# Performance work log

Hardware: AMD Instinct MI355X
Metric: run time of the kernel (lower is better)

Reference implementation:

```python
import jax, jax.numpy as jnp
import numpy as np


def setup_inputs() -> dict:
    key = jax.random.key(0)
    k1, k2, k3, k4 = jax.random.split(key, 4)
    B, C, H, W = 4, 48, 512, 512
    T, ws = 3, 64
    # factor matrices (per TensorMultiplication_einsum, T summation terms)
    # init scale: 1/(init_temperature**(1/3) * sqrt(out_dim)) with init_temperature=1.0
    Ws = jax.random.normal(k2, (T, ws, ws), jnp.float32) / np.sqrt(ws)
    Hs = jax.random.normal(k3, (T, ws, ws), jnp.float32) / np.sqrt(ws)
    Cs = jax.random.normal(k4, (T, C, C), jnp.float32) / np.sqrt(C)
    x = jax.random.normal(k1, (B, C, H, W), jnp.float32)
    return {"x": x, "Ws": Ws, "Hs": Hs, "Cs": Cs, "window_size": ws}


def reference(x, Ws, Hs, Cs, window_size):
    """FeatureProcessingBlock forward:
      window_partition -> sum_t einsum('bchw,wW,hH,cC->bCHW') -> window_reverse.
    The window partition/reverse reshapes are fused into one einsum over the
    blocked view (p,q index the window grid; h,w index within-window pixels).
    """
    B, C, H, W = x.shape
    ws = window_size
    # (B, C, H//ws, ws, W//ws, ws)
    xb = x.reshape(B, C, H // ws, ws, W // ws, ws)
    # sum over T terms and contract w, h, c axes with their factor matrices
    out = jnp.einsum('bcphqw,twW,thH,tcC->bCpHqW', xb, Ws, Hs, Cs)
    return out.reshape(B, C, H, W)
```

## Files before the change

### kernel.cpp

```cpp
#include <hip/hip_runtime.h>
#include <hip/hip_bf16.h>


typedef __attribute__((ext_vector_type(8))) short short8;
typedef __attribute__((ext_vector_type(4))) short short4v;
typedef __attribute__((ext_vector_type(4))) float float4v;

#define SMEM_BYTES 161296

static __device__ __forceinline__ unsigned short f2bf(float f) {
  return __builtin_bit_cast(unsigned short, __float2bfloat16(f));
}
static __device__ __forceinline__ unsigned int pk2(float a, float b) {
  return (unsigned int)f2bf(a) | ((unsigned int)f2bf(b) << 16);
}
static __device__ __forceinline__ void wg_barrier_lds() {
  asm volatile("s_waitcnt lgkmcnt(0)" ::: "memory");
  __builtin_amdgcn_s_barrier();
  asm volatile("" ::: "memory");
}

__global__ __launch_bounds__(512, 2)
void fpb13(const float* __restrict__ x, const float* __restrict__ Ws,
           const float* __restrict__ Hsm, const float* __restrict__ Cs,
           float* __restrict__ out) {
  extern __shared__ char smem[];
  char* Y1F = smem;
  char* Zb  = smem + 49152;
  char* Cf  = smem + 147456;
  char* z16 = smem + 161280;

  int wid = (blockIdx.x & 7) * 128 + (blockIdx.x >> 3);
  int window = wid >> 2, tile = wid & 3;
  int b = window >> 6, p = (window >> 3) & 7, q = window & 7;
  int j0 = tile * 16;

  int tid = threadIdx.x, lane = tid & 63, wave = tid >> 6;
  int lq = lane >> 4, lc = lane & 15;
  int clA = wave & 3, hh = wave >> 2;
  int mt  = wave & 3, cp = wave >> 2;

  if (tid < 4) ((unsigned int*)z16)[tid] = 0;

  for (int idx = wave; idx < 18; idx += 8) {
    int ss = idx / 3, m = idx - 3 * ss;
    if (lq < 3) {
      short8 v;
      #pragma unroll
      for (int e = 0; e < 8; ++e)
        v[e] = (short)f2bf(Cs[lq * 2304 + (8 * ss + e) * 48 + 16 * m + lc]);
      *(short8*)(Cf + (idx * 16 + lc) * 48 + lq * 16) = v;
    }
  }

  short8 wsf[3][2], hsf[3][2];
  #pragma unroll
  for (int t = 0; t < 3; ++t)
    #pragma unroll
    for (int sv = 0; sv < 2; ++sv) {
      short8 aa, bb;
      #pragma unroll
      for (int e = 0; e < 8; ++e) {
        int k = 32 * sv + 8 * lq + e;
        aa[e] = (short)f2bf(Ws [t * 4096 + k * 64 + j0 + lc]);
        bb[e] = (short)f2bf(Hsm[t * 4096 + k * 64 + 16 * mt + lc]);
      }
      wsf[t][sv] = aa; hsf[t][sv] = bb;
    }

  float4v acc[3][8];
  #pragma unroll
  for (int m = 0; m < 3; ++m)
    #pragma unroll
    for (int i = 0; i < 8; ++i) acc[m][i] = float4v{0.f, 0.f, 0.f, 0.f};

  const float* xA = x + (((size_t)b * 48) * 512 + p * 64) * 512 + q * 64
                      + (size_t)clA * 262144 + (size_t)(32 * hh + lc) * 512 + 8 * lq;

  float4v fin[8];
  #define LOADFIN(vv) do {                                        \
    const float* srcb_ = xA + (size_t)(vv) * 1048576;             \
    _Pragma("unroll")                                             \
    for (int j2_ = 0; j2_ < 2; ++j2_) {                           \
      const float* r_ = srcb_ + (size_t)j2_ * 8192;               \
      fin[4*j2_+0] = *(const float4v*)(r_);                       \
      fin[4*j2_+1] = *(const float4v*)(r_ + 4);                   \
      fin[4*j2_+2] = *(const float4v*)(r_ + 32);                  \
      fin[4*j2_+3] = *(const float4v*)(r_ + 36);                  \
    }                                                             \
  } while (0)

  #define ABLOCK(vv) do {                                                     \
    char* yb_ = Y1F + ((vv) & 1) * 24576;                                     \
    short8 af_[4];                                                            \
    _Pragma("unroll")                                                         \
    for (int j2_ = 0; j2_ < 2; ++j2_) {                                       \
      short8 a0_, a1_;                                                        \
      _Pragma("unroll")                                                       \
      for (int e2_ = 0; e2_ < 4; ++e2_) {                                     \
        a0_[e2_]   = (short)f2bf(fin[4*j2_+0][e2_]);                          \
        a0_[4+e2_] = (short)f2bf(fin[4*j2_+1][e2_]);                          \
        a1_[e2_]   = (short)f2bf(fin[4*j2_+2][e2_]);                          \
        a1_[4+e2_] = (short)f2bf(fin[4*j2_+3][e2_]);                          \
      }                                                                       \
      af_[2*j2_] = a0_; af_[2*j2_+1] = a1_;                                   \
    }                                                                         \
    if ((vv) < 11) LOADFIN((vv) + 1);                                         \
    _Pragma("unroll")                                                         \
    for (int j2_ = 0; j2_ < 2; ++j2_) {                                       \
      int mA_  = 2 * hh + j2_;                                                \
      int sv_  = mA_ >> 1;                                                    \
      int lqp_ = (2 * mA_ + (lq >> 1)) & 3;                                   \
      int eo_  = (lq & 1) * 8;                                                \
      _Pragma("unroll")                                                       \
      for (int t_ = 0; t_ < 3; ++t_) {                                        \
        float4v d_ = {0.f, 0.f, 0.f, 0.f};                                    \
        d_ = __builtin_amdgcn_mfma_f32_16x16x32_bf16(af_[2*j2_],   wsf[t_][0], d_, 0, 0, 0); \
        d_ = __builtin_amdgcn_mfma_f32_16x16x32_bf16(af_[2*j2_+1], wsf[t_][1], d_, 0, 0, 0); \
        short4v pv_;                                                          \
        pv_[0] = (short)f2bf(d_[0]); pv_[1] = (short)f2bf(d_[1]);             \
        pv_[2] = (short)f2bf(d_[2]); pv_[3] = (short)f2bf(d_[3]);             \
        *(short4v*)(yb_ + ((t_ * 4 + clA) * 2 + sv_) * 1024                   \
                        + (lqp_ * 16 + lc) * 16 + eo_) = pv_;                 \
      }                                                                       \
    }                                                                         \
  } while (0)

  LOADFIN(0);
  wg_barrier_lds();
  ABLOCK(0);
  wg_barrier_lds();

  #pragma unroll 1
  for (int v = 0; v < 12; ++v) {
    {
      const char* yb = Y1F + (v & 1) * 24576;
      char* zb = Zb + ((v >> 1) & 1) * 49152;
      int half = (v & 1) * 8;
      #pragma unroll
      for (int t = 0; t < 3; ++t) {
        float4v dB[2];
        #pragma unroll
        for (int cj = 0; cj < 2; ++cj) {
          int cl = 2 * cp + cj;
          const char* ybs = yb + ((t * 4 + cl) * 2) * 1024 + lane * 16;
          short8 y0 = *(const short8*)ybs;
          short8 y1 = *(const short8*)(ybs + 1024);
          float4v dd = {0.f, 0.f, 0.f, 0.f};
          dd = __builtin_amdgcn_mfma_f32_16x16x32_bf16(hsf[t][0], y0, dd, 0, 0, 0);
          dd = __builtin_amdgcn_mfma_f32_16x16x32_bf16(hsf[t][1], y1, dd, 0, 0, 0);
          dB[cj] = dd;
        }
        #pragma unroll
        for (int r = 0; r < 4; ++r) {
          int px = (16 * mt + 4 * lq + r) * 16 + lc;
          *(unsigned int*)(zb + t * 16384 + px * 16 + half + 4 * cp) =
              pk2(dB[0][r], dB[1][r]);
        }
      }
    }
    if (v < 11) ABLOCK(v + 1);
    if ((v & 1) && v >= 3) {
      int Sp = (v >> 1) - 1;
      const char* zb = Zb + (Sp & 1) * 49152;
      short8 cf[3];
      #pragma unroll
      for (int m = 0; m < 3; ++m) {
        const char* csrc = (lq < 3) ? (Cf + ((Sp * 3 + m) * 16 + lc) * 48 + lq * 16) : z16;
        cf[m] = *(const short8*)csrc;
      }
      #pragma unroll
      for (int i = 0; i < 8; ++i) {
        int px = 16 * (wave + 8 * i) + lc;
        const char* zsrc = (lq < 3) ? (zb + lq * 16384 + px * 16) : z16;
        short8 zf = *(const short8*)zsrc;
        acc[0][i] = __builtin_amdgcn_mfma_f32_16x16x32_bf16(cf[0], zf, acc[0][i], 0, 0, 0);
        acc[1][i] = __builtin_amdgcn_mfma_f32_16x16x32_bf16(cf[1], zf, acc[1][i], 0, 0, 0);
        acc[2][i] = __builtin_amdgcn_mfma_f32_16x16x32_bf16(cf[2], zf, acc[2][i], 0, 0, 0);
      }
    }
    wg_barrier_lds();
  }

  {
    const char* zb = Zb + 1 * 49152;
    short8 cf[3];
    #pragma unroll
    for (int m = 0; m < 3; ++m) {
      const char* csrc = (lq < 3) ? (Cf + ((5 * 3 + m) * 16 + lc) * 48 + lq * 16) : z16;
      cf[m] = *(const short8*)csrc;
    }
    #pragma unroll
    for (int i = 0; i < 8; ++i) {
      int px = 16 * (wave + 8 * i) + lc;
      const char* zsrc = (lq < 3) ? (zb + lq * 16384 + px * 16) : z16;
      short8 zf = *(const short8*)zsrc;
      acc[0][i] = __builtin_amdgcn_mfma_f32_16x16x32_bf16(cf[0], zf, acc[0][i], 0, 0, 0);
      acc[1][i] = __builtin_amdgcn_mfma_f32_16x16x32_bf16(cf[1], zf, acc[1][i], 0, 0, 0);
      acc[2][i] = __builtin_amdgcn_mfma_f32_16x16x32_bf16(cf[2], zf, acc[2][i], 0, 0, 0);
    }
  }

  #pragma unroll
  for (int m = 0; m < 3; ++m)
    #pragma unroll
    for (int i = 0; i < 8; ++i) {
      int n = wave + 8 * i;
      size_t rowbase = (((size_t)(b * 48 + 16 * m + 4 * lq)) * 512 + p * 64 + n) * 512
                       + q * 64 + j0 + lc;
      #pragma unroll
      for (int r = 0; r < 4; ++r)
        out[rowbase + (size_t)r * 262144] = acc[m][i][r];
    }
}

extern "C" void kernel_launch(void* const* d_in, const int* in_sizes, int n_in,
                              void* d_out, int out_size, void* d_ws, size_t ws_size,
                              hipStream_t stream) {
  (void)in_sizes; (void)n_in; (void)d_ws; (void)ws_size; (void)out_size;
  const float* x   = (const float*)d_in[0];
  const float* Ws  = (const float*)d_in[1];
  const float* Hsm = (const float*)d_in[2];
  const float* Cs  = (const float*)d_in[3];
  float* out = (float*)d_out;
  (void)hipFuncSetAttribute((const void*)fpb13,
                            hipFuncAttributeMaxDynamicSharedMemorySize, SMEM_BYTES);
  fpb13<<<dim3(1024), dim3(512), SMEM_BYTES, stream>>>(x, Ws, Hsm, Cs, out);
}
```

Measured before the change: 191.2 us.

## Warp-specialize waves into W-stage producers and H-stage consumers with 8-channel chunks

Splits the workgroup so waves 0-3 do the H contraction and waves 4-7 do the global load plus W contraction. Each step now handles 8 channels instead of 4, with a single Z buffer and doubled Y1 buffers. All waves still run the C contraction after a barrier. The aim is to overlap the global loads and first-stage MFMA work with the second stage while halving the number of barrier-synchronized steps. The cost is an uneven per-wave workload, more registers for the doubled fin buffers, and role-split waves sharing barriers, which may serialize work instead of overlapping it.

```diff
diff --git a/kernel.cpp b/kernel.cpp
--- a/kernel.cpp
+++ b/kernel.cpp
@@ -10,9 +10,6 @@
 
 static __device__ __forceinline__ unsigned short f2bf(float f) {
   return __builtin_bit_cast(unsigned short, __float2bfloat16(f));
-}
-static __device__ __forceinline__ unsigned int pk2(float a, float b) {
-  return (unsigned int)f2bf(a) | ((unsigned int)f2bf(b) << 16);
 }
 static __device__ __forceinline__ void wg_barrier_lds() {
   asm volatile("s_waitcnt lgkmcnt(0)" ::: "memory");
@@ -21,12 +18,12 @@
 }
 
 __global__ __launch_bounds__(512, 2)
-void fpb13(const float* __restrict__ x, const float* __restrict__ Ws,
+void fpb14(const float* __restrict__ x, const float* __restrict__ Ws,
            const float* __restrict__ Hsm, const float* __restrict__ Cs,
            float* __restrict__ out) {
   extern __shared__ char smem[];
   char* Y1F = smem;
-  char* Zb  = smem + 49152;
+  char* Zb  = smem + 98304;
   char* Cf  = smem + 147456;
   char* z16 = smem + 161280;
 
@@ -37,8 +34,6 @@
 
   int tid = threadIdx.x, lane = tid & 63, wave = tid >> 6;
   int lq = lane >> 4, lc = lane & 15;
-  int clA = wave & 3, hh = wave >> 2;
-  int mt  = wave & 3, cp = wave >> 2;
 
   if (tid < 4) ((unsigned int*)z16)[tid] = 0;
 
@@ -53,151 +48,158 @@
     }
   }
 
-  short8 wsf[3][2], hsf[3][2];
-  #pragma unroll
-  for (int t = 0; t < 3; ++t)
-    #pragma unroll
-    for (int sv = 0; sv < 2; ++sv) {
-      short8 aa, bb;
-      #pragma unroll
-      for (int e = 0; e < 8; ++e) {
-        int k = 32 * sv + 8 * lq + e;
-        aa[e] = (short)f2bf(Ws [t * 4096 + k * 64 + j0 + lc]);
-        bb[e] = (short)f2bf(Hsm[t * 4096 + k * 64 + 16 * mt + lc]);
-      }
-      wsf[t][sv] = aa; hsf[t][sv] = bb;
-    }
-
   float4v acc[3][8];
   #pragma unroll
   for (int m = 0; m < 3; ++m)
     #pragma unroll
     for (int i = 0; i < 8; ++i) acc[m][i] = float4v{0.f, 0.f, 0.f, 0.f};
 
-  const float* xA = x + (((size_t)b * 48) * 512 + p * 64) * 512 + q * 64
-                      + (size_t)clA * 262144 + (size_t)(32 * hh + lc) * 512 + 8 * lq;
-
-  float4v fin[8];
-  #define LOADFIN(vv) do {                                        \
-    const float* srcb_ = xA + (size_t)(vv) * 1048576;             \
-    _Pragma("unroll")                                             \
-    for (int j2_ = 0; j2_ < 2; ++j2_) {                           \
-      const float* r_ = srcb_ + (size_t)j2_ * 8192;               \
-      fin[4*j2_+0] = *(const float4v*)(r_);                       \
-      fin[4*j2_+1] = *(const float4v*)(r_ + 4);                   \
-      fin[4*j2_+2] = *(const float4v*)(r_ + 32);                  \
-      fin[4*j2_+3] = *(const float4v*)(r_ + 36);                  \
-    }                                                             \
-  } while (0)
-
-  #define ABLOCK(vv) do {                                                     \
-    char* yb_ = Y1F + ((vv) & 1) * 24576;                                     \
-    short8 af_[4];                                                            \
+  #define CBLOCK(s_) do {                                                     \
+    short8 cf_[3];                                                            \
     _Pragma("unroll")                                                         \
-    for (int j2_ = 0; j2_ < 2; ++j2_) {                                       \
-      short8 a0_, a1_;                                                        \
-      _Pragma("unroll")                                                       \
-      for (int e2_ = 0; e2_ < 4; ++e2_) {                                     \
-        a0_[e2_]   = (short)f2bf(fin[4*j2_+0][e2_]);                          \
-        a0_[4+e2_] = (short)f2bf(fin[4*j2_+1][e2_]);                          \
-        a1_[e2_]   = (short)f2bf(fin[4*j2_+2][e2_]);                          \
-        a1_[4+e2_] = (short)f2bf(fin[4*j2_+3][e2_]);                          \
-      }                                                                       \
-      af_[2*j2_] = a0_; af_[2*j2_+1] = a1_;                                   \
+    for (int m_ = 0; m_ < 3; ++m_) {                                          \
+      const char* cs_ = (lq < 3) ? (Cf + (((s_) * 3 + m_) * 16 + lc) * 48 + lq * 16) : z16; \
+      cf_[m_] = *(const short8*)cs_;                                          \
     }                                                                         \
-    if ((vv) < 11) LOADFIN((vv) + 1);                                         \
     _Pragma("unroll")                                                         \
-    for (int j2_ = 0; j2_ < 2; ++j2_) {                                       \
-      int mA_  = 2 * hh + j2_;                                                \
-      int sv_  = mA_ >> 1;                                                    \
-      int lqp_ = (2 * mA_ + (lq >> 1)) & 3;                                   \
-      int eo_  = (lq & 1) * 8;                                                \
-      _Pragma("unroll")                                                       \
-      for (int t_ = 0; t_ < 3; ++t_) {                                        \
-        float4v d_ = {0.f, 0.f, 0.f, 0.f};                                    \
-        d_ = __builtin_amdgcn_mfma_f32_16x16x32_bf16(af_[2*j2_],   wsf[t_][0], d_, 0, 0, 0); \
-        d_ = __builtin_amdgcn_mfma_f32_16x16x32_bf16(af_[2*j2_+1], wsf[t_][1], d_, 0, 0, 0); \
-        short4v pv_;                                                          \
-        pv_[0] = (short)f2bf(d_[0]); pv_[1] = (short)f2bf(d_[1]);             \
-        pv_[2] = (short)f2bf(d_[2]); pv_[3] = (short)f2bf(d_[3]);             \
-        *(short4v*)(yb_ + ((t_ * 4 + clA) * 2 + sv_) * 1024                   \
-                        + (lqp_ * 16 + lc) * 16 + eo_) = pv_;                 \
-      }                                                                       \
+    for (int i_ = 0; i_ < 8; ++i_) {                                          \
+      int px_ = 16 * (wave + 8 * i_) + lc;                                    \
+      const char* zs_ = (lq < 3) ? (Zb + lq * 16384 + px_ * 16) : z16;        \
+      short8 zf_ = *(const short8*)zs_;                                       \
+      acc[0][i_] = __builtin_amdgcn_mfma_f32_16x16x32_bf16(cf_[0], zf_, acc[0][i_], 0, 0, 0); \
+      acc[1][i_] = __builtin_amdgcn_mfma_f32_16x16x32_bf16(cf_[1], zf_, acc[1][i_], 0, 0, 0); \
+      acc[2][i_] = __builtin_amdgcn_mfma_f32_16x16x32_bf16(cf_[2], zf_, acc[2][i_], 0, 0, 0); \
     }                                                                         \
   } while (0)
 
-  LOADFIN(0);
-  wg_barrier_lds();
-  ABLOCK(0);
-  wg_barrier_lds();
-
-  #pragma unroll 1
-  for (int v = 0; v < 12; ++v) {
-    {
-      const char* yb = Y1F + (v & 1) * 24576;
-      char* zb = Zb + ((v >> 1) & 1) * 49152;
-      int half = (v & 1) * 8;
+  if (wave < 4) {
+    int mt = wave;
+    short8 hsf[3][2];
+    #pragma unroll
+    for (int t = 0; t < 3; ++t)
+      #pragma unroll
+      for (int sv = 0; sv < 2; ++sv) {
+        short8 bb;
+        #pragma unroll
+        for (int e = 0; e < 8; ++e)
+          bb[e] = (short)f2bf(Hsm[t * 4096 + (32 * sv + 8 * lq + e) * 64 + 16 * mt + lc]);
+        hsf[t][sv] = bb;
+      }
+    wg_barrier_lds();
+
+    #pragma unroll 1
+    for (int s = 0; s < 6; ++s) {
+      const char* yb = Y1F + (s & 1) * 49152;
       #pragma unroll
       for (int t = 0; t < 3; ++t) {
-        float4v dB[2];
-        #pragma unroll
-        for (int cj = 0; cj < 2; ++cj) {
-          int cl = 2 * cp + cj;
-          const char* ybs = yb + ((t * 4 + cl) * 2) * 1024 + lane * 16;
+        float4v dd[8];
+        #pragma unroll
+        for (int cl = 0; cl < 8; ++cl) {
+          const char* ybs = yb + ((t * 8 + cl) * 2) * 1024 + lane * 16;
           short8 y0 = *(const short8*)ybs;
           short8 y1 = *(const short8*)(ybs + 1024);
-          float4v dd = {0.f, 0.f, 0.f, 0.f};
-          dd = __builtin_amdgcn_mfma_f32_16x16x32_bf16(hsf[t][0], y0, dd, 0, 0, 0);
-          dd = __builtin_amdgcn_mfma_f32_16x16x32_bf16(hsf[t][1], y1, dd, 0, 0, 0);
-          dB[cj] = dd;
+          float4v d = {0.f, 0.f, 0.f, 0.f};
+          d = __builtin_amdgcn_mfma_f32_16x16x32_bf16(hsf[t][0], y0, d, 0, 0, 0);
+          d = __builtin_amdgcn_mfma_f32_16x16x32_bf16(hsf[t][1], y1, d, 0, 0, 0);
+          dd[cl] = d;
         }
         #pragma unroll
         for (int r = 0; r < 4; ++r) {
+          short8 v;
+          #pragma unroll
+          for (int e = 0; e < 8; ++e) v[e] = (short)f2bf(dd[e][r]);
           int px = (16 * mt + 4 * lq + r) * 16 + lc;
-          *(unsigned int*)(zb + t * 16384 + px * 16 + half + 4 * cp) =
-              pk2(dB[0][r], dB[1][r]);
+          *(short8*)(Zb + t * 16384 + px * 16) = v;
         }
       }
-    }
-    if (v < 11) ABLOCK(v + 1);
-    if ((v & 1) && v >= 3) {
-      int Sp = (v >> 1) - 1;
-      const char* zb = Zb + (Sp & 1) * 49152;
-      short8 cf[3];
-      #pragma unroll
-      for (int m = 0; m < 3; ++m) {
-        const char* csrc = (lq < 3) ? (Cf + ((Sp * 3 + m) * 16 + lc) * 48 + lq * 16) : z16;
-        cf[m] = *(const short8*)csrc;
+      wg_barrier_lds();
+      CBLOCK(s);
+      if (s < 5) wg_barrier_lds();
+    }
+  } else {
+    int aIdx = wave - 4;
+    short8 wsf[3][2];
+    #pragma unroll
+    for (int t = 0; t < 3; ++t)
+      #pragma unroll
+      for (int sv = 0; sv < 2; ++sv) {
+        short8 aa;
+        #pragma unroll
+        for (int e = 0; e < 8; ++e)
+          aa[e] = (short)f2bf(Ws[t * 4096 + (32 * sv + 8 * lq + e) * 64 + j0 + lc]);
+        wsf[t][sv] = aa;
       }
-      #pragma unroll
-      for (int i = 0; i < 8; ++i) {
-        int px = 16 * (wave + 8 * i) + lc;
-        const char* zsrc = (lq < 3) ? (zb + lq * 16384 + px * 16) : z16;
-        short8 zf = *(const short8*)zsrc;
-        acc[0][i] = __builtin_amdgcn_mfma_f32_16x16x32_bf16(cf[0], zf, acc[0][i], 0, 0, 0);
-        acc[1][i] = __builtin_amdgcn_mfma_f32_16x16x32_bf16(cf[1], zf, acc[1][i], 0, 0, 0);
-        acc[2][i] = __builtin_amdgcn_mfma_f32_16x16x32_bf16(cf[2], zf, acc[2][i], 0, 0, 0);
-      }
-    }
+
+    const float* xwin = x + (((size_t)b * 48) * 512 + p * 64) * 512 + q * 64
+                          + (size_t)lc * 512 + 8 * lq;
+    const float* xA0 = xwin + (size_t)aIdx * 262144;
+    const float* xA1 = xwin + (size_t)(aIdx + 4) * 262144;
+
+    float4v fin[2][8];
+    #define LOADQ(h_, base_, s_) do {                                          \
+      const float* r0_ = (base_) + (size_t)(s_) * 2097152 + (size_t)(32 * (h_)) * 512; \
+      fin[h_][0] = *(const float4v*)(r0_);      fin[h_][1] = *(const float4v*)(r0_ + 4); \
+      fin[h_][2] = *(const float4v*)(r0_ + 32); fin[h_][3] = *(const float4v*)(r0_ + 36); \
+      const float* r1_ = r0_ + 8192;                                           \
+      fin[h_][4] = *(const float4v*)(r1_);      fin[h_][5] = *(const float4v*)(r1_ + 4); \
+      fin[h_][6] = *(const float4v*)(r1_ + 32); fin[h_][7] = *(const float4v*)(r1_ + 36); \
+    } while (0)
+
+    #define AQUARTER(chi_, h_, s_) do {                                        \
+      short8 af_[4];                                                           \
+      _Pragma("unroll")                                                        \
+      for (int j2_ = 0; j2_ < 2; ++j2_) {                                      \
+        short8 a0_, a1_;                                                       \
+        _Pragma("unroll")                                                      \
+        for (int e2_ = 0; e2_ < 4; ++e2_) {                                    \
+          a0_[e2_]   = (short)f2bf(fin[h_][4*j2_+0][e2_]);                     \
+          a0_[4+e2_] = (short)f2bf(fin[h_][4*j2_+1][e2_]);                     \
+          a1_[e2_]   = (short)f2bf(fin[h_][4*j2_+2][e2_]);                     \
+          a1_[4+e2_] = (short)f2bf(fin[h_][4*j2_+3][e2_]);                     \
+        }                                                                      \
+        af_[2*j2_] = a0_; af_[2*j2_+1] = a1_;                                  \
+      }                                                                        \
+      if ((chi_) == 0) { LOADQ(h_, xA1, (s_)); }                               \
+      else if ((s_) < 5) { LOADQ(h_, xA0, (s_) + 1); }                         \
+      {                                                                        \
+        int ch_ = aIdx + 4 * (chi_);                                           \
+        char* ybuf_ = Y1F + ((s_) & 1) * 49152;                                \
+        _Pragma("unroll")                                                      \
+        for (int j2_ = 0; j2_ < 2; ++j2_) {                                    \
+          int mA_  = 2 * (h_) + j2_;                                           \
+          int lqp_ = (2 * mA_ + (lq >> 1)) & 3;                                \
+          int eo_  = (lq & 1) * 8;                                             \
+          _Pragma("unroll")                                                    \
+          for (int t_ = 0; t_ < 3; ++t_) {                                     \
+            float4v d_ = {0.f, 0.f, 0.f, 0.f};                                 \
+            d_ = __builtin_amdgcn_mfma_f32_16x16x32_bf16(af_[2*j2_],   wsf[t_][0], d_, 0, 0, 0); \
+            d_ = __builtin_amdgcn_mfma_f32_16x16x32_bf16(af_[2*j2_+1], wsf[t_][1], d_, 0, 0, 0); \
+            short4v pv_;                                                       \
+            pv_[0] = (short)f2bf(d_[0]); pv_[1] = (short)f2bf(d_[1]);          \
+            pv_[2] = (short)f2bf(d_[2]); pv_[3] = (short)f2bf(d_[3]);          \
+            *(short4v*)(ybuf_ + ((t_ * 8 + ch_) * 2 + (h_)) * 1024             \
+                              + (lqp_ * 16 + lc) * 16 + eo_) = pv_;            \
+          }                                                                    \
+        }                                                                      \
+      }                                                                        \
+    } while (0)
+
+    #define ABLOCK(s_) do {                                                    \
+      AQUARTER(0, 0, (s_)); AQUARTER(0, 1, (s_));                              \
+      AQUARTER(1, 0, (s_)); AQUARTER(1, 1, (s_));                              \
+    } while (0)
+
+    LOADQ(0, xA0, 0);
+    LOADQ(1, xA0, 0);
+    ABLOCK(0);
     wg_barrier_lds();
-  }
-
-  {
-    const char* zb = Zb + 1 * 49152;
-    short8 cf[3];
-    #pragma unroll
-    for (int m = 0; m < 3; ++m) {
-      const char* csrc = (lq < 3) ? (Cf + ((5 * 3 + m) * 16 + lc) * 48 + lq * 16) : z16;
-      cf[m] = *(const short8*)csrc;
-    }
-    #pragma unroll
-    for (int i = 0; i < 8; ++i) {
-      int px = 16 * (wave + 8 * i) + lc;
-      const char* zsrc = (lq < 3) ? (zb + lq * 16384 + px * 16) : z16;
-      short8 zf = *(const short8*)zsrc;
-      acc[0][i] = __builtin_amdgcn_mfma_f32_16x16x32_bf16(cf[0], zf, acc[0][i], 0, 0, 0);
-      acc[1][i] = __builtin_amdgcn_mfma_f32_16x16x32_bf16(cf[1], zf, acc[1][i], 0, 0, 0);
-      acc[2][i] = __builtin_amdgcn_mfma_f32_16x16x32_bf16(cf[2], zf, acc[2][i], 0, 0, 0);
+
+    #pragma unroll 1
+    for (int s = 0; s < 6; ++s) {
+      if (s < 5) ABLOCK(s + 1);
+      wg_barrier_lds();
+      CBLOCK(s);
+      if (s < 5) wg_barrier_lds();
     }
   }
 
@@ -223,7 +225,7 @@
   const float* Hsm = (const float*)d_in[2];
   const float* Cs  = (const float*)d_in[3];
   float* out = (float*)d_out;
-  (void)hipFuncSetAttribute((const void*)fpb13,
+  (void)hipFuncSetAttribute((const void*)fpb14,
                             hipFuncAttributeMaxDynamicSharedMemorySize, SMEM_BYTES);
-  fpb13<<<dim3(1024), dim3(512), SMEM_BYTES, stream>>>(x, Ws, Hsm, Cs, out);
-}
+  fpb14<<<dim3(1024), dim3(512), SMEM_BYTES, stream>>>(x, Ws, Hsm, Cs, out);
+}
```

After: 195.8 us. +2.4%, slower.

## Restructure pipeline into six 8-channel stages with interleaved half-block prefetch

Applied to the files above, without the earlier changes.

The main loop now runs 6 stages, each covering 8 input channels, instead of 12 stages of 4 channels. The first-contraction work for the next stage is split into two halves, interleaved with the H-contraction and the C-contraction of the current stage. The Z buffer is now a single interleaved pixel-major layout written with 64-bit packed stores, replacing the double-buffered t-major layout. This is meant to cut barrier count and loop overhead and to widen LDS stores. In exchange, it holds twice as many prefetched input registers and may add LDS bank conflicts with the 48-byte stride.

```diff
diff --git a/kernel.cpp b/kernel.cpp
--- a/kernel.cpp
+++ b/kernel.cpp
@@ -11,8 +11,10 @@
 static __device__ __forceinline__ unsigned short f2bf(float f) {
   return __builtin_bit_cast(unsigned short, __float2bfloat16(f));
 }
-static __device__ __forceinline__ unsigned int pk2(float a, float b) {
-  return (unsigned int)f2bf(a) | ((unsigned int)f2bf(b) << 16);
+static __device__ __forceinline__ unsigned long long pk4(float a, float b, float c, float d) {
+  unsigned long long lo = (unsigned int)((unsigned int)f2bf(a) | ((unsigned int)f2bf(b) << 16));
+  unsigned long long hi = (unsigned int)((unsigned int)f2bf(c) | ((unsigned int)f2bf(d) << 16));
+  return lo | (hi << 32);
 }
 static __device__ __forceinline__ void wg_barrier_lds() {
   asm volatile("s_waitcnt lgkmcnt(0)" ::: "memory");
@@ -21,12 +23,12 @@
 }
 
 __global__ __launch_bounds__(512, 2)
-void fpb13(const float* __restrict__ x, const float* __restrict__ Ws,
+void fpb15(const float* __restrict__ x, const float* __restrict__ Ws,
            const float* __restrict__ Hsm, const float* __restrict__ Cs,
            float* __restrict__ out) {
   extern __shared__ char smem[];
   char* Y1F = smem;
-  char* Zb  = smem + 49152;
+  char* Zb  = smem + 98304;
   char* Cf  = smem + 147456;
   char* z16 = smem + 161280;
 
@@ -37,8 +39,7 @@
 
   int tid = threadIdx.x, lane = tid & 63, wave = tid >> 6;
   int lq = lane >> 4, lc = lane & 15;
-  int clA = wave & 3, hh = wave >> 2;
-  int mt  = wave & 3, cp = wave >> 2;
+  int mt = wave & 3, cp = wave >> 2;
 
   if (tid < 4) ((unsigned int*)z16)[tid] = 0;
 
@@ -74,43 +75,45 @@
     #pragma unroll
     for (int i = 0; i < 8; ++i) acc[m][i] = float4v{0.f, 0.f, 0.f, 0.f};
 
-  const float* xA = x + (((size_t)b * 48) * 512 + p * 64) * 512 + q * 64
-                      + (size_t)clA * 262144 + (size_t)(32 * hh + lc) * 512 + 8 * lq;
-
-  float4v fin[8];
-  #define LOADFIN(vv) do {                                        \
-    const float* srcb_ = xA + (size_t)(vv) * 1048576;             \
-    _Pragma("unroll")                                             \
-    for (int j2_ = 0; j2_ < 2; ++j2_) {                           \
-      const float* r_ = srcb_ + (size_t)j2_ * 8192;               \
-      fin[4*j2_+0] = *(const float4v*)(r_);                       \
-      fin[4*j2_+1] = *(const float4v*)(r_ + 4);                   \
-      fin[4*j2_+2] = *(const float4v*)(r_ + 32);                  \
-      fin[4*j2_+3] = *(const float4v*)(r_ + 36);                  \
-    }                                                             \
+  const float* xbase = x + (((size_t)b * 48) * 512 + p * 64) * 512 + q * 64
+                         + (size_t)wave * 262144 + (size_t)lc * 512 + 8 * lq;
+
+  float4v fin[2][8];
+
+  #define LOADFIN(h_, s_) do {                                     \
+    const float* src_ = xbase + (size_t)(s_) * 2097152             \
+                              + (size_t)(32 * (h_)) * 512;         \
+    _Pragma("unroll")                                              \
+    for (int j2_ = 0; j2_ < 2; ++j2_) {                            \
+      const float* r_ = src_ + (size_t)(16 * j2_) * 512;           \
+      fin[h_][4*j2_+0] = *(const float4v*)(r_);                    \
+      fin[h_][4*j2_+1] = *(const float4v*)(r_ + 4);                \
+      fin[h_][4*j2_+2] = *(const float4v*)(r_ + 32);               \
+      fin[h_][4*j2_+3] = *(const float4v*)(r_ + 36);               \
+    }                                                              \
   } while (0)
 
-  #define ABLOCK(vv) do {                                                     \
-    char* yb_ = Y1F + ((vv) & 1) * 24576;                                     \
+  #define AHALF(h_, st_) do {                                                 \
+    char* ybuf_ = Y1F + ((st_) & 1) * 49152;                                  \
     short8 af_[4];                                                            \
     _Pragma("unroll")                                                         \
     for (int j2_ = 0; j2_ < 2; ++j2_) {                                       \
       short8 a0_, a1_;                                                        \
       _Pragma("unroll")                                                       \
       for (int e2_ = 0; e2_ < 4; ++e2_) {                                     \
-        a0_[e2_]   = (short)f2bf(fin[4*j2_+0][e2_]);                          \
-        a0_[4+e2_] = (short)f2bf(fin[4*j2_+1][e2_]);                          \
-        a1_[e2_]   = (short)f2bf(fin[4*j2_+2][e2_]);                          \
-        a1_[4+e2_] = (short)f2bf(fin[4*j2_+3][e2_]);                          \
+        a0_[e2_]   = (short)f2bf(fin[h_][4*j2_+0][e2_]);                      \
+        a0_[4+e2_] = (short)f2bf(fin[h_][4*j2_+1][e2_]);                      \
+        a1_[e2_]   = (short)f2bf(fin[h_][4*j2_+2][e2_]);                      \
+        a1_[4+e2_] = (short)f2bf(fin[h_][4*j2_+3][e2_]);                      \
       }                                                                       \
       af_[2*j2_] = a0_; af_[2*j2_+1] = a1_;                                   \
     }                                                                         \
-    if ((vv) < 11) LOADFIN((vv) + 1);                                         \
+    if ((st_) < 5) LOADFIN(h_, (st_) + 1);                                    \
     _Pragma("unroll")                                                         \
     for (int j2_ = 0; j2_ < 2; ++j2_) {                                       \
-      int mA_  = 2 * hh + j2_;                                                \
+      int mA_  = 2 * (h_) + j2_;                                              \
       int sv_  = mA_ >> 1;                                                    \
-      int lqp_ = (2 * mA_ + (lq >> 1)) & 3;                                   \
+      int lqp_ = (2 * mA_ + (lq >> 1)) & 3;      \
       int eo_  = (lq & 1) * 8;                                                \
       _Pragma("unroll")                                                       \
       for (int t_ = 0; t_ < 3; ++t_) {                                        \
@@ -120,30 +123,29 @@
         short4v pv_;                                                          \
         pv_[0] = (short)f2bf(d_[0]); pv_[1] = (short)f2bf(d_[1]);             \
         pv_[2] = (short)f2bf(d_[2]); pv_[3] = (short)f2bf(d_[3]);             \
-        *(short4v*)(yb_ + ((t_ * 4 + clA) * 2 + sv_) * 1024                   \
-                        + (lqp_ * 16 + lc) * 16 + eo_) = pv_;                 \
+        *(short4v*)(ybuf_ + ((t_ * 8 + wave) * 2 + sv_) * 1024                \
+                          + (lqp_ * 16 + lc) * 16 + eo_) = pv_;               \
       }                                                                       \
     }                                                                         \
   } while (0)
 
-  LOADFIN(0);
+  LOADFIN(0, 0);
+  LOADFIN(1, 0);
   wg_barrier_lds();
-  ABLOCK(0);
+  AHALF(0, 0);
+  AHALF(1, 0);
   wg_barrier_lds();
 
   #pragma unroll 1
-  for (int v = 0; v < 12; ++v) {
+  for (int s = 0; s < 6; ++s) {
     {
-      const char* yb = Y1F + (v & 1) * 24576;
-      char* zb = Zb + ((v >> 1) & 1) * 49152;
-      int half = (v & 1) * 8;
+      const char* yb = Y1F + (s & 1) * 49152;
       #pragma unroll
       for (int t = 0; t < 3; ++t) {
-        float4v dB[2];
+        float4v dB[4];
         #pragma unroll
-        for (int cj = 0; cj < 2; ++cj) {
-          int cl = 2 * cp + cj;
-          const char* ybs = yb + ((t * 4 + cl) * 2) * 1024 + lane * 16;
+        for (int cj = 0; cj < 4; ++cj) {
+          const char* ybs = yb + ((t * 8 + 4 * cp + cj) * 2) * 1024 + lane * 16;
           short8 y0 = *(const short8*)ybs;
           short8 y1 = *(const short8*)(ybs + 1024);
           float4v dd = {0.f, 0.f, 0.f, 0.f};
@@ -154,51 +156,33 @@
         #pragma unroll
         for (int r = 0; r < 4; ++r) {
           int px = (16 * mt + 4 * lq + r) * 16 + lc;
-          *(unsigned int*)(zb + t * 16384 + px * 16 + half + 4 * cp) =
-              pk2(dB[0][r], dB[1][r]);
+          *(unsigned long long*)(Zb + px * 48 + 16 * t + 8 * cp) =
+              pk4(dB[0][r], dB[1][r], dB[2][r], dB[3][r]);
         }
       }
-    }
-    if (v < 11) ABLOCK(v + 1);
-    if ((v & 1) && v >= 3) {
-      int Sp = (v >> 1) - 1;
-      const char* zb = Zb + (Sp & 1) * 49152;
+      if (s < 5) AHALF(0, s + 1);
+    }
+    wg_barrier_lds();
+
+    {
       short8 cf[3];
       #pragma unroll
       for (int m = 0; m < 3; ++m) {
-        const char* csrc = (lq < 3) ? (Cf + ((Sp * 3 + m) * 16 + lc) * 48 + lq * 16) : z16;
+        const char* csrc = (lq < 3) ? (Cf + ((s * 3 + m) * 16 + lc) * 48 + lq * 16) : z16;
         cf[m] = *(const short8*)csrc;
       }
       #pragma unroll
       for (int i = 0; i < 8; ++i) {
         int px = 16 * (wave + 8 * i) + lc;
-        const char* zsrc = (lq < 3) ? (zb + lq * 16384 + px * 16) : z16;
+        const char* zsrc = (lq < 3) ? (Zb + px * 48 + 16 * lq) : z16;
         short8 zf = *(const short8*)zsrc;
         acc[0][i] = __builtin_amdgcn_mfma_f32_16x16x32_bf16(cf[0], zf, acc[0][i], 0, 0, 0);
         acc[1][i] = __builtin_amdgcn_mfma_f32_16x16x32_bf16(cf[1], zf, acc[1][i], 0, 0, 0);
         acc[2][i] = __builtin_amdgcn_mfma_f32_16x16x32_bf16(cf[2], zf, acc[2][i], 0, 0, 0);
       }
+      if (s < 5) AHALF(1, s + 1);
     }
     wg_barrier_lds();
-  }
-
-  {
-    const char* zb = Zb + 1 * 49152;
-    short8 cf[3];
-    #pragma unroll
-    for (int m = 0; m < 3; ++m) {
-      const char* csrc = (lq < 3) ? (Cf + ((5 * 3 + m) * 16 + lc) * 48 + lq * 16) : z16;
-      cf[m] = *(const short8*)csrc;
-    }
-    #pragma unroll
-    for (int i = 0; i < 8; ++i) {
-      int px = 16 * (wave + 8 * i) + lc;
-      const char* zsrc = (lq < 3) ? (zb + lq * 16384 + px * 16) : z16;
-      short8 zf = *(const short8*)zsrc;
-      acc[0][i] = __builtin_amdgcn_mfma_f32_16x16x32_bf16(cf[0], zf, acc[0][i], 0, 0, 0);
-      acc[1][i] = __builtin_amdgcn_mfma_f32_16x16x32_bf16(cf[1], zf, acc[1][i], 0, 0, 0);
-      acc[2][i] = __builtin_amdgcn_mfma_f32_16x16x32_bf16(cf[2], zf, acc[2][i], 0, 0, 0);
-    }
   }
 
   #pragma unroll
@@ -223,7 +207,7 @@
   const float* Hsm = (const float*)d_in[2];
   const float* Cs  = (const float*)d_in[3];
   float* out = (float*)d_out;
-  (void)hipFuncSetAttribute((const void*)fpb13,
+  (void)hipFuncSetAttribute((const void*)fpb15,
                             hipFuncAttributeMaxDynamicSharedMemorySize, SMEM_BYTES);
-  fpb13<<<dim3(1024), dim3(512), SMEM_BYTES, stream>>>(x, Ws, Hsm, Cs, out);
-}
+  fpb15<<<dim3(1024), dim3(512), SMEM_BYTES, stream>>>(x, Ws, Hsm, Cs, out);
+}
```

After: 185.2 us. -3.1%, faster.
